# Performance work log

Hardware: AMD Instinct MI355X
Metric: run time of the kernel (lower is better)

## Reference

```python
import jax, jax.numpy as jnp
import numpy as np

MUL = 128
LS = [0, 1, 2]
D1 = [MUL * (2 * l + 1) for l in LS]            # per-irrep dims of x1 / out: 128, 384, 640
D2 = [2 * l + 1 for l in LS]                    # per-irrep dims of x2 (mul=1): 1, 3, 5
O1 = np.concatenate([[0], np.cumsum(D1)])       # offsets into x1 / out
O2 = np.concatenate([[0], np.cumsum(D2)])       # offsets into x2
PATHS = [(l1, l2, lo) for l1 in LS for l2 in LS for lo in LS
         if abs(l1 - l2) <= lo <= l1 + l2]      # 15 sorted 'uvw' instructions
DIM_OUT = int(sum(D1))

def _count():
    # fan-in count per output position: each 'uvw' path adds mul_1*mul_2 = 128
    c = np.zeros(DIM_OUT, dtype=np.float32)
    for (_, _, lo) in PATHS:
        c[O1[lo]:O1[lo] + D1[lo]] += MUL * 1
    return np.maximum(c, 1.0)

COUNT = jnp.asarray(_count())

def setup_inputs() -> dict:
    key = jax.random.key(0)
    ks = jax.random.split(key, 3 + len(PATHS))
    N = 16384
    inp = {
        "x1": jax.random.normal(ks[0], (N, int(sum(D1))), jnp.float32),
        "x2": jax.random.normal(ks[1], (N, int(sum(D2))), jnp.float32),
        "ws": jax.random.normal(ks[2], (len(PATHS), MUL, 1, MUL), jnp.float32),
    }
    for p, (l1, l2, lo) in enumerate(PATHS):
        inp[f"c{p}"] = jax.random.normal(ks[3 + p], (2 * l1 + 1, 2 * l2 + 1, 2 * lo + 1), jnp.float32)
    return inp

def _forward(x1, x2, ws, cs):
    N = x1.shape[0]
    out = jnp.zeros((N, DIM_OUT), x1.dtype)
    for p, (l1, l2, lo) in enumerate(PATHS):
        # s1: [N, mul1, 2l1+1]; s2: [N, mul2=1, 2l2+1]
        s1 = x1[:, int(O1[l1]):int(O1[l1] + D1[l1])].reshape(N, MUL, 2 * l1 + 1)
        s2 = x2[:, int(O2[l2]):int(O2[l2] + D2[l2])].reshape(N, 1, 2 * l2 + 1)
        # weighted CG contraction: ws[p] [u,v,w], cs[p] [i,j,k]
        contrib = jnp.einsum('uvw,ijk,zui,zvj->zwk', ws[p], cs[p], s1, s2)
        out = out.at[:, int(O1[lo]):int(O1[lo] + D1[lo])].add(contrib.reshape(N, D1[lo]))
    # fan-in (component) normalization
    return out / jnp.sqrt(COUNT)

def reference(x1, x2, ws, c0, c1, c2, c3, c4, c5, c6, c7, c8, c9, c10, c11, c12, c13, c14):
    cs = [c0, c1, c2, c3, c4, c5, c6, c7, c8, c9, c10, c11, c12, c13, c14]
    return _forward(x1, x2, ws, cs)
```

## Files before the change

kernel.cpp:

```cpp
#include <hip/hip_runtime.h>
#include <hip/hip_bf16.h>

typedef float f32x4 __attribute__((ext_vector_type(4)));
typedef short bf16x8 __attribute__((ext_vector_type(8)));

#define ZT 16
#define TL_STRIDE 136
#define TL_BUF (80 * TL_STRIDE)
#define YL_BUF 400

constexpr int cL1[15]  = {0,0,0,1,1,1,1,1,1,2,2,2,2,2,2};
constexpr int cL2[15]  = {0,1,2,0,1,1,1,2,2,0,1,1,2,2,2};
constexpr int cLO[15]  = {0,1,2,1,0,1,2,1,2,2,1,2,0,1,2};
constexpr int cCSZ[15] = {1,9,25,9,9,27,45,45,75,25,45,75,25,75,125};
constexpr int cCOFF[15]= {0,1,10,35,44,53,80,125,170,245,270,315,390,415,490};
constexpr int cO1[3] = {0,128,512};
constexpr int cO2[3] = {0,1,4};
constexpr int cX1O[3]= {0,1,4};

struct CP { const float* p[15]; };

__device__ __forceinline__ ushort f2bf(float f) {
    union { __hip_bfloat16 h; ushort u; } c;
    c.h = __float2bfloat16(f);
    return c.u;
}

__global__ void prep_w(const float* __restrict__ ws, ushort* __restrict__ wb) {
    __shared__ float lds[64 * 132];
    const int p = blockIdx.x;
    const int tid = threadIdx.x;
    const float* src = ws + (size_t)p * 16384;
    ushort* dst = wb + (size_t)p * 16384;
    for (int half = 0; half < 2; ++half) {
        for (int i = tid; i < 8192; i += 256) {
            int u = i >> 7, w = i & 127;
            lds[u * 132 + w] = src[(half * 64 + u) * 128 + w];
        }
        __syncthreads();
        for (int i = tid; i < 8192; i += 256) {
            int w = i >> 6, u = i & 63;
            dst[w * 128 + half * 64 + u] = f2bf(lds[u * 132 + w]);
        }
        __syncthreads();
    }
}

template<int P>
__device__ __forceinline__ void compute_y(int tid, const float* __restrict__ cl,
                                          const float* __restrict__ x2l,
                                          float* __restrict__ ybuf) {
    constexpr int l2 = cL2[P], lo = cLO[P];
    constexpr int d1 = 2*cL1[P]+1, d2 = 2*l2+1, dO = 2*lo+1;
    constexpr int span = d1 * dO;
    constexpr int ny = ZT * span;
    for (int idx = tid; idx < ny; idx += 256) {
        const int z = idx / span, rem = idx % span;
        const int i = rem / dO, k = rem % dO;
        float s = 0.f;
        #pragma unroll
        for (int j = 0; j < d2; ++j)
            s += cl[cCOFF[P] + (i*d2 + j)*dO + k] * x2l[z*9 + cO2[l2] + j];
        ybuf[idx] = s;
    }
}

template<int P>
__device__ __forceinline__ void path_iter(
    int tid, const ushort* __restrict__ Wb, const float* __restrict__ Wsrc, int use_prep,
    const float (&x1r)[8][9],
    float* __restrict__ yl, ushort* __restrict__ Tl,
    const float* __restrict__ cl, const float* __restrict__ x2l,
    f32x4 (&A0)[2][1], f32x4 (&A1)[2][3], f32x4 (&A2)[2][5])
{
    constexpr int l1 = cL1[P], lo = cLO[P];
    constexpr int d1 = 2*l1+1, dO = 2*lo+1;
    constexpr int span = d1 * dO;
    const int lane = tid & 63, wv = tid >> 6;

    ushort* Tcur = Tl + (P & 1) * TL_BUF;
    const float* ycur = yl + (P & 1) * YL_BUF;

    bf16x8 aP[2][4];
    if (use_prep) {
        const ushort* wp = Wb + P * 16384;
        #pragma unroll
        for (int mt = 0; mt < 2; ++mt)
        #pragma unroll
        for (int ks = 0; ks < 4; ++ks) {
            const int wrow = wv*32 + mt*16 + (lane & 15);
            const int k0   = ks*32 + ((lane >> 4) << 3);
            aP[mt][ks] = *reinterpret_cast<const bf16x8*>(wp + wrow*128 + k0);
        }
    } else {
        const float* wp = Wsrc + P * 16384;
        #pragma unroll
        for (int mt = 0; mt < 2; ++mt)
        #pragma unroll
        for (int ks = 0; ks < 4; ++ks) {
            const int wrow = wv*32 + mt*16 + (lane & 15);
            const int k0   = ks*32 + ((lane >> 4) << 3);
            bf16x8 v;
            #pragma unroll
            for (int e = 0; e < 8; ++e) v[e] = (short)f2bf(wp[(k0 + e)*128 + wrow]);
            aP[mt][ks] = v;
        }
    }

    {
        const int u = tid & 127, zh = tid >> 7;
        #pragma unroll
        for (int r = 0; r < 8; ++r) {
            const int z = 2*r + zh;
            #pragma unroll
            for (int k = 0; k < dO; ++k) {
                float s = 0.f;
                #pragma unroll
                for (int i = 0; i < d1; ++i)
                    s += x1r[r][cX1O[l1] + i] * ycur[z*span + i*dO + k];
                Tcur[(z*dO + k)*TL_STRIDE + u] = f2bf(s);
            }
        }
    }

    if constexpr (P < 14)
        compute_y<P + 1>(tid, cl, x2l, yl + ((P + 1) & 1) * YL_BUF);

    __syncthreads();

    #pragma unroll
    for (int ks = 0; ks < 4; ++ks) {
        const int k0 = ks*32 + ((lane >> 4) << 3);
        #pragma unroll
        for (int nt = 0; nt < dO; ++nt) {
            const bf16x8 b = *reinterpret_cast<const bf16x8*>(
                Tcur + (nt*16 + (lane & 15))*TL_STRIDE + k0);
            if constexpr (lo == 0) {
                A0[0][nt] = __builtin_amdgcn_mfma_f32_16x16x32_bf16(aP[0][ks], b, A0[0][nt], 0,0,0);
                A0[1][nt] = __builtin_amdgcn_mfma_f32_16x16x32_bf16(aP[1][ks], b, A0[1][nt], 0,0,0);
            } else if constexpr (lo == 1) {
                A1[0][nt] = __builtin_amdgcn_mfma_f32_16x16x32_bf16(aP[0][ks], b, A1[0][nt], 0,0,0);
                A1[1][nt] = __builtin_amdgcn_mfma_f32_16x16x32_bf16(aP[1][ks], b, A1[1][nt], 0,0,0);
            } else {
                A2[0][nt] = __builtin_amdgcn_mfma_f32_16x16x32_bf16(aP[0][ks], b, A2[0][nt], 0,0,0);
                A2[1][nt] = __builtin_amdgcn_mfma_f32_16x16x32_bf16(aP[1][ks], b, A2[1][nt], 0,0,0);
            }
        }
    }
}

template<int LO, int NT>
__device__ __forceinline__ void stage_lo(const f32x4 (&A)[2][NT], float* __restrict__ stage,
                                         int c, int wv, int rg, int cw, float scale)
{
    constexpr int dO = 2*LO + 1;
    #pragma unroll
    for (int nt = 0; nt < NT; ++nt) {
        const int col = nt*16 + cw;
        const int z = col / dO, k = col - z*dO;
        if ((z >> 2) == c) {
            #pragma unroll
            for (int mt = 0; mt < 2; ++mt) {
                const int row = wv*32 + mt*16 + rg;
                float* p = stage + (z & 3)*1152 + cO1[LO] + row*dO + k;
                #pragma unroll
                for (int r = 0; r < 4; ++r) p[r*dO] = A[mt][nt][r] * scale;
            }
        }
    }
}

__global__ __launch_bounds__(256, 2)
void tp_main(const float* __restrict__ x1, const float* __restrict__ x2,
             const float* __restrict__ wsrc, const ushort* __restrict__ wb,
             int use_prep, CP cp, float* __restrict__ out)
{
    __shared__ __align__(16) ushort Tl[2 * TL_BUF];
    __shared__ float yl[2 * YL_BUF];
    __shared__ float cl[615];
    __shared__ float x2l[ZT * 9];

    const int tid = threadIdx.x;
    const int z0 = blockIdx.x * ZT;

    #pragma unroll
    for (int p = 0; p < 15; ++p)
        for (int i = tid; i < cCSZ[p]; i += 256) cl[cCOFF[p] + i] = cp.p[p][i];
    for (int i = tid; i < ZT * 9; i += 256) x2l[i] = x2[(size_t)z0 * 9 + i];

    float x1r[8][9];
    {
        const int u = tid & 127, zh = tid >> 7;
        #pragma unroll
        for (int r = 0; r < 8; ++r) {
            const float* b = x1 + (size_t)(z0 + 2*r + zh) * 1152;
            x1r[r][0] = b[u];
            #pragma unroll
            for (int i = 0; i < 3; ++i) x1r[r][1 + i] = b[128 + u*3 + i];
            #pragma unroll
            for (int i = 0; i < 5; ++i) x1r[r][4 + i] = b[512 + u*5 + i];
        }
    }

    f32x4 A0[2][1], A1[2][3], A2[2][5];
    #pragma unroll
    for (int mt = 0; mt < 2; ++mt) {
        A0[mt][0] = (f32x4){0.f, 0.f, 0.f, 0.f};
        #pragma unroll
        for (int nt = 0; nt < 3; ++nt) A1[mt][nt] = (f32x4){0.f, 0.f, 0.f, 0.f};
        #pragma unroll
        for (int nt = 0; nt < 5; ++nt) A2[mt][nt] = (f32x4){0.f, 0.f, 0.f, 0.f};
    }

    __syncthreads();
    compute_y<0>(tid, cl, x2l, yl);
    __syncthreads();

    path_iter< 0>(tid, wb, wsrc, use_prep, x1r, yl, Tl, cl, x2l, A0, A1, A2);
    path_iter< 1>(tid, wb, wsrc, use_prep, x1r, yl, Tl, cl, x2l, A0, A1, A2);
    path_iter< 2>(tid, wb, wsrc, use_prep, x1r, yl, Tl, cl, x2l, A0, A1, A2);
    path_iter< 3>(tid, wb, wsrc, use_prep, x1r, yl, Tl, cl, x2l, A0, A1, A2);
    path_iter< 4>(tid, wb, wsrc, use_prep, x1r, yl, Tl, cl, x2l, A0, A1, A2);
    path_iter< 5>(tid, wb, wsrc, use_prep, x1r, yl, Tl, cl, x2l, A0, A1, A2);
    path_iter< 6>(tid, wb, wsrc, use_prep, x1r, yl, Tl, cl, x2l, A0, A1, A2);
    path_iter< 7>(tid, wb, wsrc, use_prep, x1r, yl, Tl, cl, x2l, A0, A1, A2);
    path_iter< 8>(tid, wb, wsrc, use_prep, x1r, yl, Tl, cl, x2l, A0, A1, A2);
    path_iter< 9>(tid, wb, wsrc, use_prep, x1r, yl, Tl, cl, x2l, A0, A1, A2);
    path_iter<10>(tid, wb, wsrc, use_prep, x1r, yl, Tl, cl, x2l, A0, A1, A2);
    path_iter<11>(tid, wb, wsrc, use_prep, x1r, yl, Tl, cl, x2l, A0, A1, A2);
    path_iter<12>(tid, wb, wsrc, use_prep, x1r, yl, Tl, cl, x2l, A0, A1, A2);
    path_iter<13>(tid, wb, wsrc, use_prep, x1r, yl, Tl, cl, x2l, A0, A1, A2);
    path_iter<14>(tid, wb, wsrc, use_prep, x1r, yl, Tl, cl, x2l, A0, A1, A2);

    const int lane = tid & 63, wv = tid >> 6;
    const int rg = (lane >> 4) << 2, cw = lane & 15;
    float* stage = (float*)Tl;
    #pragma unroll
    for (int c = 0; c < 4; ++c) {
        __syncthreads();
        stage_lo<0, 1>(A0, stage, c, wv, rg, cw, 0.05103103630798288f);
        stage_lo<1, 3>(A1, stage, c, wv, rg, cw, 0.03608439182435161f);
        stage_lo<2, 5>(A2, stage, c, wv, rg, cw, 0.03608439182435161f);
        __syncthreads();
        float4* dst = (float4*)(out + (size_t)(z0 + 4*c) * 1152);
        const float4* src = (const float4*)stage;
        #pragma unroll
        for (int it = 0; it < 5; ++it) {
            const int idx = it * 256 + tid;
            if (idx < 1152) dst[idx] = src[idx];
        }
    }
}

extern "C" void kernel_launch(void* const* d_in, const int* in_sizes, int n_in,
                              void* d_out, int out_size, void* d_ws, size_t ws_size,
                              hipStream_t stream) {
    const float* x1 = (const float*)d_in[0];
    const float* x2 = (const float*)d_in[1];
    const float* ws = (const float*)d_in[2];
    CP cp;
    for (int p = 0; p < 15; ++p) cp.p[p] = (const float*)d_in[3 + p];
    float* out = (float*)d_out;

    const int N = in_sizes[0] / 1152;
    const int use_prep = (ws_size >= (size_t)(15 * 128 * 128 * 2)) ? 1 : 0;

    if (use_prep)
        prep_w<<<15, 256, 0, stream>>>(ws, (ushort*)d_ws);
    tp_main<<<N / ZT, 256, 0, stream>>>(x1, x2, ws, (const ushort*)d_ws,
                                        use_prep, cp, out);
}
```

Baseline: 104.4 us.

## Remap T-build threads to per-wave rows with paired u and vectorized y loads

Each wave now owns 4 batch rows and each lane handles two adjacent u channels, so x1 is loaded with float2 reads and T entries are written as packed bf16 pairs. The y buffer is padded to a multiple of 4 per row so each row's y coefficients can be read as f32x4 vectors (uniform per wave, effectively broadcasts) instead of scalar LDS reads. This targets LDS read traffic and store count in the per-path T construction, at the cost of a different register layout for x1 and slightly larger y buffers.

```diff
diff --git a/kernel.cpp b/kernel.cpp
--- a/kernel.cpp
+++ b/kernel.cpp
@@ -7,7 +7,7 @@
 #define ZT 16
 #define TL_STRIDE 136
 #define TL_BUF (80 * TL_STRIDE)
-#define YL_BUF 400
+#define YL_BUF 448
 
 constexpr int cL1[15]  = {0,0,0,1,1,1,1,1,1,2,2,2,2,2,2};
 constexpr int cL2[15]  = {0,1,2,0,1,1,1,2,2,0,1,1,2,2,2};
@@ -53,14 +53,17 @@
     constexpr int l2 = cL2[P], lo = cLO[P];
     constexpr int d1 = 2*cL1[P]+1, d2 = 2*l2+1, dO = 2*lo+1;
     constexpr int span = d1 * dO;
-    constexpr int ny = ZT * span;
+    constexpr int span_pad = (span + 3) & ~3;
+    constexpr int ny = ZT * span_pad;
     for (int idx = tid; idx < ny; idx += 256) {
-        const int z = idx / span, rem = idx % span;
-        const int i = rem / dO, k = rem % dO;
+        const int z = idx / span_pad, rem = idx - z * span_pad;
         float s = 0.f;
-        #pragma unroll
-        for (int j = 0; j < d2; ++j)
-            s += cl[cCOFF[P] + (i*d2 + j)*dO + k] * x2l[z*9 + cO2[l2] + j];
+        if (rem < span) {
+            const int i = rem / dO, k = rem - i * dO;
+            #pragma unroll
+            for (int j = 0; j < d2; ++j)
+                s += cl[cCOFF[P] + (i*d2 + j)*dO + k] * x2l[z*9 + cO2[l2] + j];
+        }
         ybuf[idx] = s;
     }
 }
@@ -68,7 +71,7 @@
 template<int P>
 __device__ __forceinline__ void path_iter(
     int tid, const ushort* __restrict__ Wb, const float* __restrict__ Wsrc, int use_prep,
-    const float (&x1r)[8][9],
+    const float (&x1r)[4][2][9],
     float* __restrict__ yl, ushort* __restrict__ Tl,
     const float* __restrict__ cl, const float* __restrict__ x2l,
     f32x4 (&A0)[2][1], f32x4 (&A1)[2][3], f32x4 (&A2)[2][5])
@@ -76,6 +79,7 @@
     constexpr int l1 = cL1[P], lo = cLO[P];
     constexpr int d1 = 2*l1+1, dO = 2*lo+1;
     constexpr int span = d1 * dO;
+    constexpr int span_pad = (span + 3) & ~3;
     const int lane = tid & 63, wv = tid >> 6;
 
     ushort* Tcur = Tl + (P & 1) * TL_BUF;
@@ -108,17 +112,29 @@
     }
 
     {
-        const int u = tid & 127, zh = tid >> 7;
-        #pragma unroll
-        for (int r = 0; r < 8; ++r) {
-            const int z = 2*r + zh;
+        const int u0 = 2 * lane;
+        #pragma unroll
+        for (int r = 0; r < 4; ++r) {
+            const int z = wv * 4 + r;
+            f32x4 yv[span_pad / 4];
+            #pragma unroll
+            for (int j = 0; j < span_pad / 4; ++j)
+                yv[j] = *reinterpret_cast<const f32x4*>(ycur + z * span_pad + 4 * j);
             #pragma unroll
             for (int k = 0; k < dO; ++k) {
-                float s = 0.f;
+                float s0 = 0.f, s1 = 0.f;
                 #pragma unroll
-                for (int i = 0; i < d1; ++i)
-                    s += x1r[r][cX1O[l1] + i] * ycur[z*span + i*dO + k];
-                Tcur[(z*dO + k)*TL_STRIDE + u] = f2bf(s);
+                for (int i = 0; i < d1; ++i) {
+                    constexpr int base = 0;  (void)base;
+                    const int yi = i * dO + k;
+                    const float yf = yv[yi >> 2][yi & 3];
+                    s0 += x1r[r][0][cX1O[l1] + i] * yf;
+                    s1 += x1r[r][1][cX1O[l1] + i] * yf;
+                }
+                union { uint u32; ushort h[2]; } pk;
+                pk.h[0] = f2bf(s0);
+                pk.h[1] = f2bf(s1);
+                *reinterpret_cast<uint*>(Tcur + (z * dO + k) * TL_STRIDE + u0) = pk.u32;
             }
         }
     }
@@ -176,29 +192,46 @@
              int use_prep, CP cp, float* __restrict__ out)
 {
     __shared__ __align__(16) ushort Tl[2 * TL_BUF];
-    __shared__ float yl[2 * YL_BUF];
+    __shared__ __align__(16) float yl[2 * YL_BUF];
     __shared__ float cl[615];
     __shared__ float x2l[ZT * 9];
 
     const int tid = threadIdx.x;
     const int z0 = blockIdx.x * ZT;
+    const int lane = tid & 63, wv = tid >> 6;
 
     #pragma unroll
     for (int p = 0; p < 15; ++p)
         for (int i = tid; i < cCSZ[p]; i += 256) cl[cCOFF[p] + i] = cp.p[p][i];
     for (int i = tid; i < ZT * 9; i += 256) x2l[i] = x2[(size_t)z0 * 9 + i];
 
-    float x1r[8][9];
-    {
-        const int u = tid & 127, zh = tid >> 7;
-        #pragma unroll
-        for (int r = 0; r < 8; ++r) {
-            const float* b = x1 + (size_t)(z0 + 2*r + zh) * 1152;
-            x1r[r][0] = b[u];
-            #pragma unroll
-            for (int i = 0; i < 3; ++i) x1r[r][1 + i] = b[128 + u*3 + i];
-            #pragma unroll
-            for (int i = 0; i < 5; ++i) x1r[r][4 + i] = b[512 + u*5 + i];
+    float x1r[4][2][9];
+    #pragma unroll
+    for (int r = 0; r < 4; ++r) {
+        const float* b = x1 + (size_t)(z0 + wv*4 + r) * 1152;
+        {
+            const float2 t = *reinterpret_cast<const float2*>(b + 2*lane);
+            x1r[r][0][0] = t.x; x1r[r][1][0] = t.y;
+        }
+        {
+            float f6[6];
+            #pragma unroll
+            for (int j = 0; j < 3; ++j) {
+                const float2 t = *reinterpret_cast<const float2*>(b + 128 + 6*lane + 2*j);
+                f6[2*j] = t.x; f6[2*j + 1] = t.y;
+            }
+            #pragma unroll
+            for (int i = 0; i < 3; ++i) { x1r[r][0][1+i] = f6[i]; x1r[r][1][1+i] = f6[3+i]; }
+        }
+        {
+            float f10[10];
+            #pragma unroll
+            for (int j = 0; j < 5; ++j) {
+                const float2 t = *reinterpret_cast<const float2*>(b + 512 + 10*lane + 2*j);
+                f10[2*j] = t.x; f10[2*j + 1] = t.y;
+            }
+            #pragma unroll
+            for (int i = 0; i < 5; ++i) { x1r[r][0][4+i] = f10[i]; x1r[r][1][4+i] = f10[5+i]; }
         }
     }
 
@@ -232,7 +265,6 @@
     path_iter<13>(tid, wb, wsrc, use_prep, x1r, yl, Tl, cl, x2l, A0, A1, A2);
     path_iter<14>(tid, wb, wsrc, use_prep, x1r, yl, Tl, cl, x2l, A0, A1, A2);
 
-    const int lane = tid & 63, wv = tid >> 6;
     const int rg = (lane >> 4) << 2, cw = lane & 15;
     float* stage = (float*)Tl;
     #pragma unroll
```

Measured after the change: 93.52 us. -10.4%, faster.
